# Optimization experiments

Hardware: AMD Instinct MI355X
Metric: run time of the kernel (lower is better)

## Reference

```python
import jax, jax.numpy as jnp
import numpy as np

SEQ, B, I, H = 1024, 64, 256, 256

def setup_inputs() -> dict:
    key = jax.random.key(0)
    k1, k2, k3 = jax.random.split(key, 3)
    # xavier-ish scale for the weights to keep gates in a sane range
    s_ih = float(np.sqrt(6.0 / (I + H)))
    s_hh = float(np.sqrt(6.0 / (H + H)))
    return {
        "inputs": jax.random.normal(k1, (SEQ, B, I), dtype=jnp.float32),
        "weight_ih": jax.random.normal(k2, (8, I, H), dtype=jnp.float32) * s_ih,
        "weight_hh": jax.random.normal(k3, (8, H, H), dtype=jnp.float32) * s_hh,
    }

def _nas_rnn(inputs, weight_ih, weight_hh):
    S, Bb, _ = inputs.shape
    Hh = weight_hh.shape[-1]
    # precompute input projections for all 8 gates: [S, 8, B, H]
    ihs = jnp.einsum("sbi,gih->sgbh", inputs, weight_ih)

    def step(carry, ih):
        state_c, state_m = carry  # each [B, H]
        hh = jnp.einsum("bh,ghk->gbk", state_m, weight_hh)  # [8, B, H]
        g = ih + hh  # [8, B, H]
        l1_0 = jax.nn.sigmoid(g[0])
        l1_1 = jax.nn.relu(g[1])
        l1_2 = jax.nn.sigmoid(g[2])
        l1_3 = jax.nn.relu(g[3])
        l1_4 = jnp.tanh(g[4])
        l1_5 = jax.nn.sigmoid(g[5])
        l1_6 = jnp.tanh(g[6])
        l1_7 = jax.nn.sigmoid(g[7])
        l2_0 = jnp.tanh(l1_0 * l1_1)
        l2_1 = jnp.tanh(l1_2 + l1_3)
        l2_2 = jnp.tanh(l1_4 * l1_5)
        l2_3 = jax.nn.sigmoid(l1_6 + l1_7)
        l2_0_v2 = jnp.tanh(l2_0 + state_c)
        new_c = l2_0_v2 * l2_1
        l3_1 = jnp.tanh(l2_2 + l2_3)
        new_m = jnp.tanh(new_c * l3_1)
        return (new_c, new_m), None

    init = (jnp.zeros((Bb, Hh), jnp.float32), jnp.zeros((Bb, Hh), jnp.float32))
    (state_c, state_m), _ = jax.lax.scan(step, init, ihs)
    return state_c + state_m

def reference(inputs, weight_ih, weight_hh):
    return _nas_rnn(inputs, weight_ih, weight_hh)
```

## Files before the change

kernel.cpp:

```cpp
#include <hip/hip_runtime.h>

#define SEQ 1024
#define NB  64
#define NI  256
#define NH  256

typedef __bf16 bf16x8 __attribute__((ext_vector_type(8)));
typedef float  f32x4  __attribute__((ext_vector_type(4)));
typedef unsigned int u32x4 __attribute__((ext_vector_type(4)));
typedef unsigned short u16;
typedef unsigned int u32;

static __device__ __forceinline__ u16 f2bf(float f) {
    u32 u = __float_as_uint(f);
    u += 0x7fffu + ((u >> 16) & 1u);
    return (u16)(u >> 16);
}
static __device__ __forceinline__ float sigm_(float x) {
    return __builtin_amdgcn_rcpf(1.0f + __builtin_amdgcn_exp2f(-1.4426950408889634f * x));
}
static __device__ __forceinline__ float tanh_(float x) {
    return 1.0f - 2.0f * __builtin_amdgcn_rcpf(__builtin_amdgcn_exp2f(2.8853900817779268f * x) + 1.0f);
}

static __device__ __forceinline__ void mfma_ab(f32x4& c, bf16x8 a, bf16x8 b) {
    asm("v_mfma_f32_16x16x32_bf16 %0, %1, %2, %0" : "+v"(c) : "v"(a), "a"(b));
}

static __device__ __forceinline__ void st_mall_u32(u32* p, u32 v) {
    asm volatile("global_store_dword %0, %1, off sc0 sc1" :: "v"(p), "v"(v) : "memory");
}

#define PREFETCH8(dst, p)                                                    \
    asm volatile(                                                            \
        "global_load_dwordx4 %0, %8, off\n\t"                                \
        "global_load_dwordx4 %1, %8, off offset:16\n\t"                      \
        "global_load_dwordx4 %2, %8, off offset:32\n\t"                      \
        "global_load_dwordx4 %3, %8, off offset:48\n\t"                      \
        "global_load_dwordx4 %4, %8, off offset:64\n\t"                      \
        "global_load_dwordx4 %5, %8, off offset:80\n\t"                      \
        "global_load_dwordx4 %6, %8, off offset:96\n\t"                      \
        "global_load_dwordx4 %7, %8, off offset:112"                         \
        : "=&v"(dst[0]), "=&v"(dst[1]), "=&v"(dst[2]), "=&v"(dst[3]),        \
          "=&v"(dst[4]), "=&v"(dst[5]), "=&v"(dst[6]), "=&v"(dst[7])         \
        : "v"(p) : "memory")

#define BAR_LGKM() do {                                                      \
    asm volatile("s_waitcnt lgkmcnt(0)" ::: "memory");                       \
    __builtin_amdgcn_s_barrier();                                            \
    __builtin_amdgcn_sched_barrier(0); } while (0)

__global__ __launch_bounds__(256, 1) __attribute__((amdgpu_waves_per_eu(1, 1)))
void nas_scan(const float* __restrict__ xg, const float* __restrict__ wih,
              const float* __restrict__ whh, float* __restrict__ out,
              u32* ctl, u32* mex)
{
    __shared__ __align__(16) unsigned char xbuf[32 * 512];
    __shared__ __align__(16) unsigned char mstage[32 * 512];
    __shared__ float gbuf[32 * 133];
    __shared__ int sh_group, sh_role;

    const int t    = threadIdx.x;
    const int lane = t & 63;
    const int wave = t >> 6;

    if (t == 0) {
        u32 xcc;
        asm volatile("s_getreg_b32 %0, hwreg(HW_REG_XCC_ID)" : "=s"(xcc));
        int grp = -1, rl = -1;
        for (int gq = 0; gq < 2 && grp < 0; ++gq) {
            u32 exp = 0u;
            bool won = __hip_atomic_compare_exchange_strong(
                &ctl[gq], &exp, xcc + 1u,
                __ATOMIC_ACQ_REL, __ATOMIC_ACQUIRE, __HIP_MEMORY_SCOPE_AGENT);
            u32 ldr = won ? (xcc + 1u) : exp;
            if (ldr == xcc + 1u) {
                u32 r = __hip_atomic_fetch_add(&ctl[2 + gq], 1u,
                                               __ATOMIC_RELAXED, __HIP_MEMORY_SCOPE_AGENT);
                if (r < 16u) { grp = gq; rl = (int)r; }
            }
        }
        sh_group = grp; sh_role = rl;
    }
    __syncthreads();
    const int g = sh_group;
    if (g < 0) return;
    const int role = sh_role;
    const int c0   = role * 16;

    const int fr = lane & 15;
    const int fq = lane >> 4;

    bf16x8 wfih[2][8], wfhh[2][8];
#pragma unroll
    for (int gi = 0; gi < 2; ++gi) {
        const int gg = wave * 2 + gi;
#pragma unroll
        for (int ks = 0; ks < 8; ++ks) {
            bf16x8 a, b;
#pragma unroll
            for (int j = 0; j < 8; ++j) {
                const int idx = (gg * NH + ks * 32 + fq * 8 + j) * NH + (c0 + fr);
                a[j] = (__bf16)wih[idx];
                b[j] = (__bf16)whh[idx];
            }
            wfih[gi][ks] = a;
            wfhh[gi][ks] = b;
        }
    }
#pragma unroll
    for (int gi = 0; gi < 2; ++gi)
#pragma unroll
        for (int ks = 0; ks < 8; ++ks)
            asm volatile("" : "+a"(wfih[gi][ks]), "+a"(wfhh[gi][ks]));

    const int xr  = t >> 3;
    const int xcb = (t & 7) * 32;
    const float* xbase = xg + (size_t)(g * 32 + xr) * NI + xcb;
    const unsigned sbase = (unsigned)xr * 512u + (unsigned)xcb * 2u;
    const unsigned sswz  = ((unsigned)xr & 7u) << 4;

    f32x4 xpA[8], xpB[8];
#pragma unroll
    for (int i = 0; i < 8; ++i) xpA[i] = *(const f32x4*)(xbase + i * 4);
    {
        u32 w[16];
#pragma unroll
        for (int jj = 0; jj < 16; ++jj) {
            const float a = xpA[jj >> 1][(jj & 1) * 2 + 0];
            const float b = xpA[jj >> 1][(jj & 1) * 2 + 1];
            w[jj] = (u32)f2bf(a) | ((u32)f2bf(b) << 16);
        }
#pragma unroll
        for (int q = 0; q < 4; ++q) {
            u32x4 W = {w[q * 4 + 0], w[q * 4 + 1], w[q * 4 + 2], w[q * 4 + 3]};
            *(u32x4*)(xbuf + ((sbase + (unsigned)q * 16u) ^ sswz)) = W;
        }
    }
    __syncthreads();

    const unsigned aswz = ((unsigned)fr & 7u) << 4;
    const unsigned ab0  = (unsigned)fr * 512u + (unsigned)fq * 16u;
    const unsigned ab1  = ab0 + 16u * 512u;

    const f32x4 fzero = {0.f, 0.f, 0.f, 0.f};
    f32x4 accx[2][2];
#pragma unroll
    for (int m = 0; m < 2; ++m)
#pragma unroll
        for (int gi = 0; gi < 2; ++gi) accx[m][gi] = fzero;
#pragma unroll
    for (int ks = 0; ks < 8; ++ks) {
        bf16x8 a0 = *(const bf16x8*)(xbuf + ((ab0 + (unsigned)ks * 64u) ^ aswz));
        bf16x8 a1 = *(const bf16x8*)(xbuf + ((ab1 + (unsigned)ks * 64u) ^ aswz));
#pragma unroll
        for (int gi = 0; gi < 2; ++gi) {
            mfma_ab(accx[0][gi], a0, wfih[gi][ks]);
            mfma_ab(accx[1][gi], a1, wfih[gi][ks]);
        }
    }
#pragma unroll
    for (int i = 0; i < 8; ++i) xpA[i] = *(const f32x4*)(xbase + (size_t)(NB * NI) + i * 4);

    const int r_own = t >> 3;
    const int cp    = t & 7;
    float cA = 0.0f, cB = 0.0f;

#define STEP(S_, XPC, XPN) do {                                               \
    const int s = (S_);                                                       \
    f32x4 acc[2][2];                                                          \
    _Pragma("unroll")                                                         \
    for (int m = 0; m < 2; ++m)                                               \
        _Pragma("unroll")                                                     \
        for (int gi = 0; gi < 2; ++gi) acc[m][gi] = accx[m][gi];              \
    if (s > 0) {                                                              \
                     \
        const u32 txor = (s & 2) ? 0x40004000u : 0u;                          \
        const u32* mp = mex + (size_t)((s & 1) * 2 + g) * 4096 + (size_t)t * 16; \
        u32x4 w0, w1, w2, w3;                                                 \
        for (;;) {                                                            \
            asm volatile(                                                     \
                "global_load_dwordx4 %0, %4, off sc0 sc1\n\t"                 \
                "global_load_dwordx4 %1, %4, off offset:16 sc0 sc1\n\t"       \
                "global_load_dwordx4 %2, %4, off offset:32 sc0 sc1\n\t"       \
                "global_load_dwordx4 %3, %4, off offset:48 sc0 sc1\n\t"       \
                "s_waitcnt vmcnt(0)"                                          \
                : "=&v"(w0), "=&v"(w1), "=&v"(w2), "=&v"(w3)                  \
                : "v"(mp) : "memory");                                        \
            u32 bad = 0u;                                                     \
            _Pragma("unroll")                                                 \
            for (int q = 0; q < 4; ++q) {                                     \
                bad |= (w0[q] ^ txor); bad |= (w1[q] ^ txor);                 \
                bad |= (w2[q] ^ txor); bad |= (w3[q] ^ txor);                 \
            }                                                                 \
            if (__all((int)((bad & 0x40004000u) == 0u))) break;               \
        }                                                                     \
        {                         \
            const int sp = (s + 2 < SEQ) ? s + 2 : s;                         \
            const float* xq = xbase + (size_t)sp * (NB * NI);                 \
            PREFETCH8(XPN, xq);                                               \
        }                                                                     \
        {                          \
            const unsigned mo  = (unsigned)t * 64u;                           \
            const unsigned msw = ((unsigned)(t >> 3) & 7u) << 4;              \
            u32x4 q0 = {w0[0] & 0xBFFFBFFFu, w0[1] & 0xBFFFBFFFu,             \
                        w0[2] & 0xBFFFBFFFu, w0[3] & 0xBFFFBFFFu};            \
            u32x4 q1 = {w1[0] & 0xBFFFBFFFu, w1[1] & 0xBFFFBFFFu,             \
                        w1[2] & 0xBFFFBFFFu, w1[3] & 0xBFFFBFFFu};            \
            u32x4 q2 = {w2[0] & 0xBFFFBFFFu, w2[1] & 0xBFFFBFFFu,             \
                        w2[2] & 0xBFFFBFFFu, w2[3] & 0xBFFFBFFFu};            \
            u32x4 q3 = {w3[0] & 0xBFFFBFFFu, w3[1] & 0xBFFFBFFFu,             \
                        w3[2] & 0xBFFFBFFFu, w3[3] & 0xBFFFBFFFu};            \
            *(u32x4*)(mstage + ((mo + 0u)  ^ msw)) = q0;                      \
            *(u32x4*)(mstage + ((mo + 16u) ^ msw)) = q1;                      \
            *(u32x4*)(mstage + ((mo + 32u) ^ msw)) = q2;                      \
            *(u32x4*)(mstage + ((mo + 48u) ^ msw)) = q3;                      \
        }                                                                     \
        BAR_LGKM();                                                           \
        _Pragma("unroll")                                                     \
        for (int ks = 0; ks < 8; ++ks) {                                      \
            bf16x8 a0 = *(const bf16x8*)(mstage + ((ab0 + (unsigned)ks * 64u) ^ aswz)); \
            bf16x8 a1 = *(const bf16x8*)(mstage + ((ab1 + (unsigned)ks * 64u) ^ aswz)); \
            _Pragma("unroll")                                                 \
            for (int gi = 0; gi < 2; ++gi) {                                  \
                mfma_ab(acc[0][gi], a0, wfhh[gi][ks]);                        \
                mfma_ab(acc[1][gi], a1, wfhh[gi][ks]);                        \
            }                                                                 \
        }                                                                     \
    } else {                                                                  \
        const float* xq = xbase + (size_t)2 * (NB * NI);                      \
        PREFETCH8(XPN, xq);                                                   \
    }                                                                         \
    _Pragma("unroll")                                                         \
    for (int m = 0; m < 2; ++m)                                               \
        _Pragma("unroll")                                                     \
        for (int gi = 0; gi < 2; ++gi) {                                      \
            const int colw = (wave * 2 + gi) * 16 + fr;                       \
            _Pragma("unroll")                                                 \
            for (int j = 0; j < 4; ++j)                                       \
                gbuf[(m * 16 + fq * 4 + j) * 133 + colw] = acc[m][gi][j];     \
        }                                                                     \
    BAR_LGKM();                                                               \
    float nm0, nm1;                                                           \
    {                                                                         \
        float nc[2], nm[2];                                                   \
        const float* gb = gbuf + r_own * 133 + cp * 2;                        \
        _Pragma("unroll")                                                     \
        for (int e = 0; e < 2; ++e) {                                         \
            const float q0 = gb[0 * 16 + e], q1 = gb[1 * 16 + e];             \
            const float q2 = gb[2 * 16 + e], q3 = gb[3 * 16 + e];             \
            const float q4 = gb[4 * 16 + e], q5 = gb[5 * 16 + e];             \
            const float q6 = gb[6 * 16 + e], q7 = gb[7 * 16 + e];             \
            const float l10 = sigm_(q0);                                      \
            const float l11 = fmaxf(q1, 0.0f);                                \
            const float l12 = sigm_(q2);                                      \
            const float l13 = fmaxf(q3, 0.0f);                                \
            const float l14 = tanh_(q4);                                      \
            const float l15 = sigm_(q5);                                      \
            const float l16 = tanh_(q6);                                      \
            const float l17 = sigm_(q7);                                      \
            const float l20 = tanh_(l10 * l11);                               \
            const float l21 = tanh_(l12 + l13);                               \
            const float l22 = tanh_(l14 * l15);                               \
            const float l23 = sigm_(l16 + l17);                               \
            const float cold = (e == 0) ? cA : cB;                            \
            const float l20v = tanh_(l20 + cold);                             \
            const float ncv  = l20v * l21;                                    \
            const float l31  = tanh_(l22 + l23);                              \
            nc[e] = ncv;                                                      \
            nm[e] = tanh_(ncv * l31);                                         \
        }                                                                     \
        cA = nc[0]; cB = nc[1];                                               \
        nm0 = nm[0]; nm1 = nm[1];                                             \
    }                                                                         \
    if (s == SEQ - 1) {                                                       \
        const int obase = (g * 32 + r_own) * NH + c0 + cp * 2;                \
        out[obase + 0] = cA + nm0;                                            \
        out[obase + 1] = cB + nm1;                                            \
    } else {                                                                  \
        \
        \
        const u32 tb = ((u32)(s + 1) & 2u) << 13;                             \
        u32* mw = mex + (size_t)(((s + 1) & 1) * 2 + g) * 4096                \
                      + (size_t)(r_own * 128 + role * 8 + cp);                \
        const u32 pk = ((u32)f2bf(nm0) | tb)                                  \
                     | ((((u32)f2bf(nm1)) | tb) << 16);                       \
        st_mall_u32(mw, pk);                                                  \
        {                                                                     \
            u32 w[16];                                                        \
            _Pragma("unroll")                                                 \
            for (int jj = 0; jj < 16; ++jj) {                                 \
                const float a = XPC[jj >> 1][(jj & 1) * 2 + 0];               \
                const float b = XPC[jj >> 1][(jj & 1) * 2 + 1];               \
                w[jj] = (u32)f2bf(a) | ((u32)f2bf(b) << 16);                  \
            }                                                                 \
            _Pragma("unroll")                                                 \
            for (int q = 0; q < 4; ++q) {                                     \
                u32x4 W = {w[q * 4 + 0], w[q * 4 + 1], w[q * 4 + 2], w[q * 4 + 3]}; \
                *(u32x4*)(xbuf + ((sbase + (unsigned)q * 16u) ^ sswz)) = W;   \
            }                                                                 \
        }                                                                     \
        BAR_LGKM();                                                           \
        _Pragma("unroll")                                                     \
        for (int m = 0; m < 2; ++m)                                           \
            _Pragma("unroll")                                                 \
            for (int gi = 0; gi < 2; ++gi) accx[m][gi] = fzero;               \
        _Pragma("unroll")                                                     \
        for (int ks = 0; ks < 8; ++ks) {                                      \
            bf16x8 a0 = *(const bf16x8*)(xbuf + ((ab0 + (unsigned)ks * 64u) ^ aswz)); \
            bf16x8 a1 = *(const bf16x8*)(xbuf + ((ab1 + (unsigned)ks * 64u) ^ aswz)); \
            _Pragma("unroll")                                                 \
            for (int gi = 0; gi < 2; ++gi) {                                  \
                mfma_ab(accx[0][gi], a0, wfih[gi][ks]);                       \
                mfma_ab(accx[1][gi], a1, wfih[gi][ks]);                       \
            }                                                                 \
        }                                                                     \
    }                                                                         \
} while (0)

    for (int sb = 0; sb < SEQ; sb += 2) {
        STEP(sb,     xpA, xpB);
        STEP(sb + 1, xpB, xpA);
    }
#undef STEP
}

__global__ void nas_init(u32* ctl, u32* mex) {
    const int b = blockIdx.x, t = threadIdx.x;
    if (b < 16) {
        const u32 v = (b < 8) ? 0u : 0x40004000u;
        u32x4 vv = {v, v, v, v};
        u32* p = mex + (size_t)b * 1024 + (size_t)t * 4;
        asm volatile("global_store_dwordx4 %0, %1, off sc0 sc1" :: "v"(p), "v"(vv) : "memory");
    } else if (t < 16) {
        u32* p = ctl + t;
        asm volatile("global_store_dword %0, %1, off sc0 sc1" :: "v"(p), "v"(0u) : "memory");
    }
}

extern "C" void kernel_launch(void* const* d_in, const int* in_sizes, int n_in,
                              void* d_out, int out_size, void* d_ws, size_t ws_size,
                              hipStream_t stream) {
    (void)in_sizes; (void)n_in; (void)out_size; (void)ws_size;
    const float* x   = (const float*)d_in[0];
    const float* wih = (const float*)d_in[1];
    const float* whh = (const float*)d_in[2];
    float* out = (float*)d_out;

    u32* ctl = (u32*)d_ws;
    u32* mex = (u32*)((char*)d_ws + 4096);

    nas_init<<<dim3(17), dim3(256), 0, stream>>>(ctl, mex);
    nas_scan<<<dim3(256), dim3(256), 0, stream>>>(x, wih, whh, out, ctl, mex);
}
```

Before: 2.606 ms.

## Load exchanged hidden state directly into MFMA operand registers, prefetched early

Each thread now loads the exchanged bf16 hidden state from global memory straight into the register layout the MFMA operand needs. This removes the LDS staging buffer and one barrier per step. The polling loads are issued right after the previous step's store and barrier, so the fetch overlaps the input-projection MFMAs, and they are re-issued only when the parity-flag check fails. The MFMA operand order is swapped (weights as A, state as B) with a matching transposed gbuf write. In exchange, each thread holds 16 more vector registers and issues more, smaller strided global loads.

Measured after the change: 3.867 ms. +48.4%, slower.

```diff
diff --git a/kernel.cpp b/kernel.cpp
--- a/kernel.cpp
+++ b/kernel.cpp
@@ -23,12 +23,16 @@
     return 1.0f - 2.0f * __builtin_amdgcn_rcpf(__builtin_amdgcn_exp2f(2.8853900817779268f * x) + 1.0f);
 }
 
-static __device__ __forceinline__ void mfma_ab(f32x4& c, bf16x8 a, bf16x8 b) {
-    asm("v_mfma_f32_16x16x32_bf16 %0, %1, %2, %0" : "+v"(c) : "v"(a), "a"(b));
+static __device__ __forceinline__ void mfma_wd(f32x4& c, bf16x8 w, bf16x8 d) {
+    asm("v_mfma_f32_16x16x32_bf16 %0, %1, %2, %0" : "+v"(c) : "a"(w), "v"(d));
 }
 
 static __device__ __forceinline__ void st_mall_u32(u32* p, u32 v) {
     asm volatile("global_store_dword %0, %1, off sc0 sc1" :: "v"(p), "v"(v) : "memory");
+}
+
+static __device__ __forceinline__ bf16x8 asbf(u32x4 v) {
+    union { u32x4 u; bf16x8 b; } c; c.u = v; return c.b;
 }
 
 #define PREFETCH8(dst, p)                                                    \
@@ -45,6 +49,37 @@
           "=&v"(dst[4]), "=&v"(dst[5]), "=&v"(dst[6]), "=&v"(dst[7])         \
         : "v"(p) : "memory")
 
+#define ISSUE16(MP) do {                                                     \
+    asm volatile(                                                            \
+        "global_load_dwordx4 %0, %8, off sc0 sc1\n\t"                        \
+        "global_load_dwordx4 %1, %8, off offset:64 sc0 sc1\n\t"              \
+        "global_load_dwordx4 %2, %8, off offset:128 sc0 sc1\n\t"             \
+        "global_load_dwordx4 %3, %8, off offset:192 sc0 sc1\n\t"             \
+        "global_load_dwordx4 %4, %8, off offset:256 sc0 sc1\n\t"             \
+        "global_load_dwordx4 %5, %8, off offset:320 sc0 sc1\n\t"             \
+        "global_load_dwordx4 %6, %8, off offset:384 sc0 sc1\n\t"             \
+        "global_load_dwordx4 %7, %8, off offset:448 sc0 sc1"                 \
+        : "=&v"(mwv[0]), "=&v"(mwv[1]), "=&v"(mwv[2]), "=&v"(mwv[3]),        \
+          "=&v"(mwv[4]), "=&v"(mwv[5]), "=&v"(mwv[6]), "=&v"(mwv[7])         \
+        : "v"(MP) : "memory");                                               \
+    asm volatile(                                                            \
+        "global_load_dwordx4 %0, %8, off sc0 sc1\n\t"                        \
+        "global_load_dwordx4 %1, %8, off offset:64 sc0 sc1\n\t"              \
+        "global_load_dwordx4 %2, %8, off offset:128 sc0 sc1\n\t"             \
+        "global_load_dwordx4 %3, %8, off offset:192 sc0 sc1\n\t"             \
+        "global_load_dwordx4 %4, %8, off offset:256 sc0 sc1\n\t"             \
+        "global_load_dwordx4 %5, %8, off offset:320 sc0 sc1\n\t"             \
+        "global_load_dwordx4 %6, %8, off offset:384 sc0 sc1\n\t"             \
+        "global_load_dwordx4 %7, %8, off offset:448 sc0 sc1"                 \
+        : "=&v"(mwv[8]),  "=&v"(mwv[9]),  "=&v"(mwv[10]), "=&v"(mwv[11]),    \
+          "=&v"(mwv[12]), "=&v"(mwv[13]), "=&v"(mwv[14]), "=&v"(mwv[15])     \
+        : "v"((MP) + 2048) : "memory");                                      \
+} while (0)
+
+#define VMWAIT() do {                                                        \
+    asm volatile("s_waitcnt vmcnt(0)" ::: "memory");                         \
+    __builtin_amdgcn_sched_barrier(0); } while (0)
+
 #define BAR_LGKM() do {                                                      \
     asm volatile("s_waitcnt lgkmcnt(0)" ::: "memory");                       \
     __builtin_amdgcn_s_barrier();                                            \
@@ -56,7 +91,6 @@
               u32* ctl, u32* mex)
 {
     __shared__ __align__(16) unsigned char xbuf[32 * 512];
-    __shared__ __align__(16) unsigned char mstage[32 * 512];
     __shared__ float gbuf[32 * 133];
     __shared__ int sh_group, sh_role;
 
@@ -155,8 +189,8 @@
         bf16x8 a1 = *(const bf16x8*)(xbuf + ((ab1 + (unsigned)ks * 64u) ^ aswz));
 #pragma unroll
         for (int gi = 0; gi < 2; ++gi) {
-            mfma_ab(accx[0][gi], a0, wfih[gi][ks]);
-            mfma_ab(accx[1][gi], a1, wfih[gi][ks]);
+            mfma_wd(accx[0][gi], wfih[gi][ks], a0);
+            mfma_wd(accx[1][gi], wfih[gi][ks], a1);
         }
     }
 #pragma unroll
@@ -165,6 +199,8 @@
     const int r_own = t >> 3;
     const int cp    = t & 7;
     float cA = 0.0f, cB = 0.0f;
+
+    u32x4 mwv[16];
 
 #define STEP(S_, XPC, XPN) do {                                               \
     const int s = (S_);                                                       \
@@ -174,71 +210,55 @@
         _Pragma("unroll")                                                     \
         for (int gi = 0; gi < 2; ++gi) acc[m][gi] = accx[m][gi];              \
     if (s > 0) {                                                              \
-                     \
         const u32 txor = (s & 2) ? 0x40004000u : 0u;                          \
-        const u32* mp = mex + (size_t)((s & 1) * 2 + g) * 4096 + (size_t)t * 16; \
-        u32x4 w0, w1, w2, w3;                                                 \
+        const u32* mp = mex + (size_t)((s & 1) * 2 + g) * 4096                \
+                      + (size_t)(fr * 128 + fq * 4);                          \
         for (;;) {                                                            \
-            asm volatile(                                                     \
-                "global_load_dwordx4 %0, %4, off sc0 sc1\n\t"                 \
-                "global_load_dwordx4 %1, %4, off offset:16 sc0 sc1\n\t"       \
-                "global_load_dwordx4 %2, %4, off offset:32 sc0 sc1\n\t"       \
-                "global_load_dwordx4 %3, %4, off offset:48 sc0 sc1\n\t"       \
-                "s_waitcnt vmcnt(0)"                                          \
-                : "=&v"(w0), "=&v"(w1), "=&v"(w2), "=&v"(w3)                  \
-                : "v"(mp) : "memory");                                        \
-            u32 bad = 0u;                                                     \
-            _Pragma("unroll")                                                 \
-            for (int q = 0; q < 4; ++q) {                                     \
-                bad |= (w0[q] ^ txor); bad |= (w1[q] ^ txor);                 \
-                bad |= (w2[q] ^ txor); bad |= (w3[q] ^ txor);                 \
-            }                                                                 \
-            if (__all((int)((bad & 0x40004000u) == 0u))) break;               \
-        }                                                                     \
-        {                         \
+            VMWAIT();                                                         \
+            u32 badw = 0u;                                                    \
+            _Pragma("unroll")                                                 \
+            for (int i = 0; i < 16; ++i)                                      \
+                badw |= (mwv[i][0] ^ txor) | (mwv[i][1] ^ txor)               \
+                      | (mwv[i][2] ^ txor) | (mwv[i][3] ^ txor);              \
+            if (__all((int)((badw & 0x40004000u) == 0u))) break;              \
+            ISSUE16(mp);                                                      \
+        }                                                                     \
+        if (s & 2) {          \
+            _Pragma("unroll")                                                 \
+            for (int i = 0; i < 16; ++i) {                                    \
+                mwv[i][0] &= 0xBFFFBFFFu; mwv[i][1] &= 0xBFFFBFFFu;           \
+                mwv[i][2] &= 0xBFFFBFFFu; mwv[i][3] &= 0xBFFFBFFFu;           \
+            }                                                                 \
+        }                                                                     \
+        {                                                \
             const int sp = (s + 2 < SEQ) ? s + 2 : s;                         \
             const float* xq = xbase + (size_t)sp * (NB * NI);                 \
             PREFETCH8(XPN, xq);                                               \
         }                                                                     \
-        {                          \
-            const unsigned mo  = (unsigned)t * 64u;                           \
-            const unsigned msw = ((unsigned)(t >> 3) & 7u) << 4;              \
-            u32x4 q0 = {w0[0] & 0xBFFFBFFFu, w0[1] & 0xBFFFBFFFu,             \
-                        w0[2] & 0xBFFFBFFFu, w0[3] & 0xBFFFBFFFu};            \
-            u32x4 q1 = {w1[0] & 0xBFFFBFFFu, w1[1] & 0xBFFFBFFFu,             \
-                        w1[2] & 0xBFFFBFFFu, w1[3] & 0xBFFFBFFFu};            \
-            u32x4 q2 = {w2[0] & 0xBFFFBFFFu, w2[1] & 0xBFFFBFFFu,             \
-                        w2[2] & 0xBFFFBFFFu, w2[3] & 0xBFFFBFFFu};            \
-            u32x4 q3 = {w3[0] & 0xBFFFBFFFu, w3[1] & 0xBFFFBFFFu,             \
-                        w3[2] & 0xBFFFBFFFu, w3[3] & 0xBFFFBFFFu};            \
-            *(u32x4*)(mstage + ((mo + 0u)  ^ msw)) = q0;                      \
-            *(u32x4*)(mstage + ((mo + 16u) ^ msw)) = q1;                      \
-            *(u32x4*)(mstage + ((mo + 32u) ^ msw)) = q2;                      \
-            *(u32x4*)(mstage + ((mo + 48u) ^ msw)) = q3;                      \
-        }                                                                     \
-        BAR_LGKM();                                                           \
         _Pragma("unroll")                                                     \
         for (int ks = 0; ks < 8; ++ks) {                                      \
-            bf16x8 a0 = *(const bf16x8*)(mstage + ((ab0 + (unsigned)ks * 64u) ^ aswz)); \
-            bf16x8 a1 = *(const bf16x8*)(mstage + ((ab1 + (unsigned)ks * 64u) ^ aswz)); \
+            const bf16x8 b0 = asbf(mwv[ks]);                                  \
+            const bf16x8 b1 = asbf(mwv[8 + ks]);                              \
             _Pragma("unroll")                                                 \
             for (int gi = 0; gi < 2; ++gi) {                                  \
-                mfma_ab(acc[0][gi], a0, wfhh[gi][ks]);                        \
-                mfma_ab(acc[1][gi], a1, wfhh[gi][ks]);                        \
+                mfma_wd(acc[0][gi], wfhh[gi][ks], b0);                        \
+                mfma_wd(acc[1][gi], wfhh[gi][ks], b1);                        \
             }                                                                 \
         }                                                                     \
     } else {                                                                  \
         const float* xq = xbase + (size_t)2 * (NB * NI);                      \
         PREFETCH8(XPN, xq);                                                   \
     }                                                                         \
+     \
     _Pragma("unroll")                                                         \
     for (int m = 0; m < 2; ++m)                                               \
         _Pragma("unroll")                                                     \
         for (int gi = 0; gi < 2; ++gi) {                                      \
-            const int colw = (wave * 2 + gi) * 16 + fr;                       \
+            const int rowb = m * 16 + fr;                                     \
+            const int colh = (wave * 2 + gi) * 16 + fq * 4;                   \
             _Pragma("unroll")                                                 \
             for (int j = 0; j < 4; ++j)                                       \
-                gbuf[(m * 16 + fq * 4 + j) * 133 + colw] = acc[m][gi][j];     \
+                gbuf[rowb * 133 + colh + j] = acc[m][gi][j];                  \
         }                                                                     \
     BAR_LGKM();                                                               \
     float nm0, nm1;                                                           \
@@ -278,15 +298,14 @@
         out[obase + 0] = cA + nm0;                                            \
         out[obase + 1] = cB + nm1;                                            \
     } else {                                                                  \
-        \
-        \
+                              \
         const u32 tb = ((u32)(s + 1) & 2u) << 13;                             \
         u32* mw = mex + (size_t)(((s + 1) & 1) * 2 + g) * 4096                \
                       + (size_t)(r_own * 128 + role * 8 + cp);                \
         const u32 pk = ((u32)f2bf(nm0) | tb)                                  \
                      | ((((u32)f2bf(nm1)) | tb) << 16);                       \
         st_mall_u32(mw, pk);                                                  \
-        {                                                                     \
+        {                                                   \
             u32 w[16];                                                        \
             _Pragma("unroll")                                                 \
             for (int jj = 0; jj < 16; ++jj) {                                 \
@@ -301,6 +320,11 @@
             }                                                                 \
         }                                                                     \
         BAR_LGKM();                                                           \
+        {   \
+            const u32* np = mex + (size_t)(((s + 1) & 1) * 2 + g) * 4096      \
+                          + (size_t)(fr * 128 + fq * 4);                      \
+            ISSUE16(np);                                                      \
+        }                                                                     \
         _Pragma("unroll")                                                     \
         for (int m = 0; m < 2; ++m)                                           \
             _Pragma("unroll")                                                 \
@@ -311,8 +335,8 @@
             bf16x8 a1 = *(const bf16x8*)(xbuf + ((ab1 + (unsigned)ks * 64u) ^ aswz)); \
             _Pragma("unroll")                                                 \
             for (int gi = 0; gi < 2; ++gi) {                                  \
-                mfma_ab(accx[0][gi], a0, wfih[gi][ks]);                       \
-                mfma_ab(accx[1][gi], a1, wfih[gi][ks]);                       \
+                mfma_wd(accx[0][gi], wfih[gi][ks], a0);                       \
+                mfma_wd(accx[1][gi], wfih[gi][ks], a1);                       \
             }                                                                 \
         }                                                                     \
     }                                                                         \
```
